# Optimization experiments

Hardware: AMD Instinct MI355X
Metric: run time of the kernel (lower is better)

Reference implementation:

```python
import jax, jax.numpy as jnp
import numpy as np

N_NODES = 50000
N_EDGES = 1600000
H = 128
F_IN = 128
N_CLASSES = 40
N_LAYERS = 8
BETA = 0.1
C_MIN = 0.2
RESIDUAL_WEIGHT = C_MIN - BETA  # 0.1


def setup_inputs() -> dict:
    key = jax.random.key(0)
    ks = jax.random.split(key, 8)
    x = jax.random.normal(ks[0], (N_NODES, F_IN), dtype=jnp.float32)
    edge_index = jax.random.randint(ks[1], (2, N_EDGES), 0, N_NODES, dtype=jnp.int64)
    W_in = jax.random.normal(ks[2], (F_IN, H), dtype=jnp.float32) * 0.05
    b_in = jax.random.normal(ks[3], (H,), dtype=jnp.float32) * 0.05
    gcn_W = jax.random.normal(ks[4], (N_LAYERS, H, H), dtype=jnp.float32) * 0.05
    srelu_b = jax.random.normal(ks[5], (N_LAYERS, H), dtype=jnp.float32) * 0.05
    W_out = jax.random.normal(ks[6], (H, N_CLASSES), dtype=jnp.float32) * 0.05
    b_out = jax.random.normal(ks[7], (N_CLASSES,), dtype=jnp.float32) * 0.05
    return {"x": x, "edge_index": edge_index, "W_in": W_in, "b_in": b_in,
            "gcn_W": gcn_W, "srelu_b": srelu_b, "W_out": W_out, "b_out": b_out}


def _gcn_norm(edge_index, num_nodes, dtype):
    # add_remaining_self_loops: drop existing self loops (zero their weight,
    # keeping static shapes) and append a full set of self loops with weight 1.
    row, col = edge_index[0], edge_index[1]
    w = jnp.where(row == col, 0.0, 1.0).astype(dtype)
    loops = jnp.arange(num_nodes, dtype=edge_index.dtype)
    row_f = jnp.concatenate([row, loops])
    col_f = jnp.concatenate([col, loops])
    w_f = jnp.concatenate([w, jnp.ones((num_nodes,), dtype=dtype)])
    deg = jax.ops.segment_sum(w_f, row_f, num_segments=num_nodes)
    deg_inv_sqrt = jnp.where(deg > 0, deg, 1.0) ** -0.5
    deg_inv_sqrt = jnp.where(deg > 0, deg_inv_sqrt, 0.0)
    norm = deg_inv_sqrt[row_f] * w_f * deg_inv_sqrt[col_f]
    return row_f, col_f, norm


def reference(x, edge_index, W_in, b_in, gcn_W, srelu_b, W_out, b_out):
    n = x.shape[0]
    row_f, col_f, norm = _gcn_norm(edge_index, n, x.dtype)
    # input layer (eval mode: dropout is identity)
    h = jax.nn.relu(x @ W_in + b_in)
    x0 = h

    def layer(h, params):
        W, sb = params
        # degree-normalized gather -> scale -> scatter_add (aggr='add')
        agg = jax.ops.segment_sum(norm[:, None] * h[row_f], col_f, num_segments=n)
        h2 = (1.0 - RESIDUAL_WEIGHT - BETA) * agg + RESIDUAL_WEIGHT * h + BETA * x0
        h2 = h2 @ W
        # SReLU: relu(x - b) + b
        h2 = jax.nn.relu(h2 - sb) + sb
        return h2, None

    h, _ = jax.lax.scan(layer, h, (gcn_W, srelu_b))
    return h @ W_out + b_out
```

## Files before the change

kernel.cpp:

```cpp
#include <hip/hip_runtime.h>

#define N_NODES 50000
#define N_EDGES 1600000
#define HDIM 128
#define N_CLASSES 40
#define N_LAYERS 8
#define CAP 128

#define BUILD_BLOCKS 782
#define CONV_BLOCKS  3125
#define PREP_BLOCKS   600

typedef _Float16 f16;
typedef _Float16 f16x2 __attribute__((ext_vector_type(2)));
typedef _Float16 f16x4 __attribute__((ext_vector_type(4)));
typedef _Float16 f16x8 __attribute__((ext_vector_type(8)));
typedef float f32x4 __attribute__((ext_vector_type(4)));
typedef int i32x4 __attribute__((ext_vector_type(4)));

__device__ __forceinline__ int clamp_idx(int v) {
    v = v < 0 ? 0 : v;
    return v >= N_NODES ? N_NODES - 1 : v;
}


__global__ __launch_bounds__(256) void setup_kernel(
        const int* __restrict__ ei, const float* __restrict__ x,
        const float* __restrict__ W_in, const float* __restrict__ gcn_W,
        const float* __restrict__ W_out,
        int* __restrict__ deg_cnt, int* __restrict__ col_cnt,
        unsigned short* __restrict__ e_slot,
        f16* __restrict__ x16, f16* __restrict__ wt, f16* __restrict__ wot) {
    int b = blockIdx.x;
    if (b < BUILD_BLOCKS) {
        int t = b * 256 + threadIdx.x;
        if (t < N_EDGES / 8) {
            i32x4 ra = ((const i32x4*)ei)[2 * t];
            i32x4 rb = ((const i32x4*)ei)[2 * t + 1];
            i32x4 ca = ((const i32x4*)(ei + N_EDGES))[2 * t];
            i32x4 cb = ((const i32x4*)(ei + N_EDGES))[2 * t + 1];
            int rs[8] = {ra[0], ra[1], ra[2], ra[3], rb[0], rb[1], rb[2], rb[3]};
            int cs[8] = {ca[0], ca[1], ca[2], ca[3], cb[0], cb[1], cb[2], cb[3]};
#pragma unroll
            for (int i = 0; i < 8; ++i) {
                int r = clamp_idx(rs[i]);
                int c = clamp_idx(cs[i]);
                if (r != c) {
                    atomicAdd(&deg_cnt[r], 1);
                    int s = atomicAdd(&col_cnt[c], 1);
                    if (s < CAP) e_slot[(size_t)c * CAP + s] = (unsigned short)r;
                }
            }
        }
    } else if (b < BUILD_BLOCKS + CONV_BLOCKS) {
        int i = (b - BUILD_BLOCKS) * 256 + threadIdx.x;
        if (i < N_NODES * HDIM / 8) {
            const float4* xs = (const float4*)x;
            float4 v0 = xs[2 * i], v1 = xs[2 * i + 1];
            f16x8 o;
            o[0] = (f16)v0.x; o[1] = (f16)v0.y; o[2] = (f16)v0.z; o[3] = (f16)v0.w;
            o[4] = (f16)v1.x; o[5] = (f16)v1.y; o[6] = (f16)v1.z; o[7] = (f16)v1.w;
            ((f16x8*)x16)[i] = o;
        }
    } else {
        int idx = (b - BUILD_BLOCKS - CONV_BLOCKS) * 256 + threadIdx.x;
        if (idx < 9 * HDIM * HDIM) {
            int mat = idx >> 14;
            int rem = idx & 16383;
            int k = rem >> 7, n = rem & 127;
            float v = (mat == 0) ? W_in[rem] : gcn_W[(mat - 1) * 16384 + rem];
            wt[mat * 16384 + n * 128 + k] = (f16)v;
        } else {
            int j = idx - 9 * HDIM * HDIM;
            if (j < 48 * 128) {
                int n = j >> 7, k = j & 127;
                wot[n * 128 + k] = (n < N_CLASSES) ? (f16)W_out[k * N_CLASSES + n] : (f16)0.f;
            }
        }
    }
}

__global__ void combo_kernel(const int* __restrict__ deg_cnt, float4* __restrict__ combo) {
    int i = blockIdx.x * blockDim.x + threadIdx.x;
    if (i >= N_NODES) return;
    float d = (float)(deg_cnt[i] + 1);
    float dis = rsqrtf(d);
    float g = sqrtf(d);
    combo[i] = make_float4(dis, 0.8f * dis, (0.8f / d + 0.1f) * g, g);
}


__global__ __launch_bounds__(256) void agg_combine(
        const f16* __restrict__ hs, const f16* __restrict__ h0_16,
        const int* __restrict__ col_cnt, const unsigned short* __restrict__ e_slot,
        const float4* __restrict__ combo, f16* __restrict__ p16) {
    int w = (blockIdx.x * blockDim.x + threadIdx.x) >> 6;
    int lane = threadIdx.x & 63;
    if (w >= N_NODES) return;
    int cnt = col_cnt[w]; if (cnt > CAP) cnt = CAP;
    const f16x2* hp = (const f16x2*)hs;
    const unsigned short* slots = e_slot + (size_t)w * CAP;
    float ax = 0.f, ay = 0.f;
    int e = 0;
    for (; e + 8 <= cnt; e += 8) {
        ushort4 sa = *(const ushort4*)(slots + e);
        ushort4 sb = *(const ushort4*)(slots + e + 4);
        f16x2 v0 = hp[(size_t)sa.x * 64 + lane];
        f16x2 v1 = hp[(size_t)sa.y * 64 + lane];
        f16x2 v2 = hp[(size_t)sa.z * 64 + lane];
        f16x2 v3 = hp[(size_t)sa.w * 64 + lane];
        f16x2 v4 = hp[(size_t)sb.x * 64 + lane];
        f16x2 v5 = hp[(size_t)sb.y * 64 + lane];
        f16x2 v6 = hp[(size_t)sb.z * 64 + lane];
        f16x2 v7 = hp[(size_t)sb.w * 64 + lane];
        ax += (float)v0[0] + (float)v1[0] + (float)v2[0] + (float)v3[0]
            + (float)v4[0] + (float)v5[0] + (float)v6[0] + (float)v7[0];
        ay += (float)v0[1] + (float)v1[1] + (float)v2[1] + (float)v3[1]
            + (float)v4[1] + (float)v5[1] + (float)v6[1] + (float)v7[1];
    }
    for (; e + 4 <= cnt; e += 4) {
        ushort4 s4 = *(const ushort4*)(slots + e);
        f16x2 v0 = hp[(size_t)s4.x * 64 + lane];
        f16x2 v1 = hp[(size_t)s4.y * 64 + lane];
        f16x2 v2 = hp[(size_t)s4.z * 64 + lane];
        f16x2 v3 = hp[(size_t)s4.w * 64 + lane];
        ax += (float)v0[0] + (float)v1[0] + (float)v2[0] + (float)v3[0];
        ay += (float)v0[1] + (float)v1[1] + (float)v2[1] + (float)v3[1];
    }
    for (; e < cnt; ++e) {
        int r = slots[e];
        f16x2 v = hp[(size_t)r * 64 + lane];
        ax += (float)v[0];
        ay += (float)v[1];
    }
    float4 cb = combo[w];
    f16x2 hw = hp[(size_t)w * 64 + lane];
    f16x2 h0v = ((const f16x2*)h0_16)[(size_t)w * 64 + lane];
    float px = cb.y * ax + cb.z * (float)hw[0] + 0.1f * (float)h0v[0];
    float py = cb.y * ay + cb.z * (float)hw[1] + 0.1f * (float)h0v[1];
    f16x2 o; o[0] = (f16)px; o[1] = (f16)py;
    ((f16x2*)p16)[(size_t)w * 64 + lane] = o;
}

#define WT_OFF 16384

__global__ __launch_bounds__(256, 2) void gemm_mfma(
        const f16* __restrict__ A, const f16* __restrict__ Wt,
        const float* __restrict__ bvec, const float4* __restrict__ combo,
        f16* __restrict__ hs_out, f16* __restrict__ h0_out, int mode) {
    __shared__ uint4 smem4[3072];
    char* smem = (char*)smem4;
    int tid = threadIdx.x;
    int r0 = blockIdx.x * 64;

    const uint4* Asrc = (const uint4*)A;
    for (int c = tid; c < 1024; c += 256) {
        int row = c >> 4, q = c & 15;
        int grow = r0 + row; if (grow >= N_NODES) grow = N_NODES - 1;
        uint4 v = Asrc[(size_t)grow * 16 + q];
        *(uint4*)&smem[row * 256 + ((q * 16) ^ ((row & 7) << 4))] = v;
    }
    const uint4* Wsrc = (const uint4*)Wt;
    for (int c = tid; c < 2048; c += 256) {
        int n = c >> 4, q = c & 15;
        uint4 v = Wsrc[n * 16 + q];
        *(uint4*)&smem[WT_OFF + n * 256 + ((q * 16) ^ ((n & 7) << 4))] = v;
    }
    __syncthreads();

    int l = tid & 63, w = tid >> 6;
    int wr = w >> 1, wc = w & 1;
    int lg = l >> 4, lm = l & 15;

    union F8 { f16x8 v8; struct { f16x4 lo, hi; } p; };
    f32x4 acc[2][4];
#pragma unroll
    for (int m = 0; m < 2; ++m)
#pragma unroll
        for (int j = 0; j < 4; ++j) acc[m][j] = (f32x4){0.f, 0.f, 0.f, 0.f};

#pragma unroll
    for (int kk = 0; kk < 4; ++kk) {
        int boff = kk * 64 + lg * 8;
        F8 a[2], b[4];
#pragma unroll
        for (int m = 0; m < 2; ++m) {
            int row = wr * 32 + m * 16 + lm;
            int swz = (row & 7) << 4;
            int rb = row * 256;
            a[m].p.lo = *(const f16x4*)&smem[rb + (boff ^ swz)];
            a[m].p.hi = *(const f16x4*)&smem[rb + ((boff + 32) ^ swz)];
        }
#pragma unroll
        for (int j = 0; j < 4; ++j) {
            int n = wc * 64 + j * 16 + lm;
            int swz = (n & 7) << 4;
            int nb = WT_OFF + n * 256;
            b[j].p.lo = *(const f16x4*)&smem[nb + (boff ^ swz)];
            b[j].p.hi = *(const f16x4*)&smem[nb + ((boff + 32) ^ swz)];
        }
#pragma unroll
        for (int m = 0; m < 2; ++m)
#pragma unroll
            for (int j = 0; j < 4; ++j)
                acc[m][j] = __builtin_amdgcn_mfma_f32_16x16x32_f16(a[m].v8, b[j].v8, acc[m][j], 0, 0, 0);
    }

#pragma unroll
    for (int m = 0; m < 2; ++m) {
#pragma unroll
        for (int r = 0; r < 4; ++r) {
            int row = r0 + wr * 32 + m * 16 + lg * 4 + r;
            if (row < N_NODES) {
                float dis = combo[row].x;
#pragma unroll
                for (int j = 0; j < 4; ++j) {
                    int col = wc * 64 + j * 16 + lm;
                    float bias = bvec[col];
                    float v = acc[m][j][r];
                    v = mode ? fmaxf(v, bias) : fmaxf(v + bias, 0.f);
                    if (mode == 0) h0_out[(size_t)row * HDIM + col] = (f16)v;
                    hs_out[(size_t)row * HDIM + col] = (f16)(dis * v);
                }
            }
        }
    }
}

#define WOT_OFF 16384

__global__ __launch_bounds__(256) void out_mfma(
        const f16* __restrict__ A, const f16* __restrict__ Wot,
        const float* __restrict__ bo, const float4* __restrict__ combo,
        float* __restrict__ out) {
    __shared__ uint4 smem4[1792];
    char* smem = (char*)smem4;
    int tid = threadIdx.x;
    int r0 = blockIdx.x * 64;

    const uint4* Asrc = (const uint4*)A;
    for (int c = tid; c < 1024; c += 256) {
        int row = c >> 4, q = c & 15;
        int grow = r0 + row; if (grow >= N_NODES) grow = N_NODES - 1;
        uint4 v = Asrc[(size_t)grow * 16 + q];
        *(uint4*)&smem[row * 256 + ((q * 16) ^ ((row & 7) << 4))] = v;
    }
    const uint4* Wsrc = (const uint4*)Wot;
    for (int c = tid; c < 768; c += 256) {
        int n = c >> 4, q = c & 15;
        uint4 v = Wsrc[n * 16 + q];
        *(uint4*)&smem[WOT_OFF + n * 256 + ((q * 16) ^ ((n & 7) << 4))] = v;
    }
    __syncthreads();

    int l = tid & 63, w = tid >> 6;
    int lg = l >> 4, lm = l & 15;

    union F8 { f16x8 v8; struct { f16x4 lo, hi; } p; };
    f32x4 acc[3];
#pragma unroll
    for (int j = 0; j < 3; ++j) acc[j] = (f32x4){0.f, 0.f, 0.f, 0.f};

#pragma unroll
    for (int kk = 0; kk < 4; ++kk) {
        int boff = kk * 64 + lg * 8;
        F8 a, b[3];
        int row = w * 16 + lm;
        int swz = (row & 7) << 4;
        int rb = row * 256;
        a.p.lo = *(const f16x4*)&smem[rb + (boff ^ swz)];
        a.p.hi = *(const f16x4*)&smem[rb + ((boff + 32) ^ swz)];
#pragma unroll
        for (int j = 0; j < 3; ++j) {
            int n = j * 16 + lm;
            int swz2 = (n & 7) << 4;
            int nb = WOT_OFF + n * 256;
            b[j].p.lo = *(const f16x4*)&smem[nb + (boff ^ swz2)];
            b[j].p.hi = *(const f16x4*)&smem[nb + ((boff + 32) ^ swz2)];
        }
#pragma unroll
        for (int j = 0; j < 3; ++j)
            acc[j] = __builtin_amdgcn_mfma_f32_16x16x32_f16(a.v8, b[j].v8, acc[j], 0, 0, 0);
    }

#pragma unroll
    for (int r = 0; r < 4; ++r) {
        int row = r0 + w * 16 + lg * 4 + r;
        if (row < N_NODES) {
            float g2 = combo[row].w;
#pragma unroll
            for (int j = 0; j < 3; ++j) {
                int col = j * 16 + lm;
                if (col < N_CLASSES)
                    out[(size_t)row * N_CLASSES + col] = g2 * acc[j][r] + bo[col];
            }
        }
    }
}


extern "C" void kernel_launch(void* const* d_in, const int* in_sizes, int n_in,
                              void* d_out, int out_size, void* d_ws, size_t ws_size,
                              hipStream_t stream) {
    const float* x       = (const float*)d_in[0];
    const int*   ei      = (const int*)d_in[1];
    const float* W_in    = (const float*)d_in[2];
    const float* b_in    = (const float*)d_in[3];
    const float* gcn_W   = (const float*)d_in[4];
    const float* srelu_b = (const float*)d_in[5];
    const float* W_out   = (const float*)d_in[6];
    const float* b_out   = (const float*)d_in[7];
    float* outp = (float*)d_out;

    char* ws = (char*)d_ws;
    size_t off = 0;
    auto alloc = [&](size_t bytes) -> void* {
        void* p = ws + off;
        off += (bytes + 255) & ~(size_t)255;
        return p;
    };
    int*    deg_cnt = (int*)alloc((size_t)N_NODES * 4);
    int*    col_cnt = (int*)alloc((size_t)N_NODES * 4);
    float4* combo   = (float4*)alloc((size_t)N_NODES * 16);
    unsigned short* e_slot = (unsigned short*)alloc((size_t)N_NODES * CAP * 2);
    f16*    wt16    = (f16*)alloc((size_t)9 * HDIM * HDIM * 2);
    f16*    wot16   = (f16*)alloc((size_t)48 * HDIM * 2);
    f16*    x16     = (f16*)alloc((size_t)N_NODES * HDIM * 2);
    f16*    h0_16   = (f16*)alloc((size_t)N_NODES * HDIM * 2);
    f16*    hs0     = (f16*)alloc((size_t)N_NODES * HDIM * 2);
    f16*    hsA     = (f16*)alloc((size_t)N_NODES * HDIM * 2);
    f16*    hsB     = (f16*)alloc((size_t)N_NODES * HDIM * 2);
    f16*    p16     = (f16*)alloc((size_t)N_NODES * HDIM * 2);

    hipMemsetAsync(deg_cnt, 0, (size_t)N_NODES * 4, stream);
    hipMemsetAsync(col_cnt, 0, (size_t)N_NODES * 4, stream);

    setup_kernel<<<BUILD_BLOCKS + CONV_BLOCKS + PREP_BLOCKS, 256, 0, stream>>>(
        ei, x, W_in, gcn_W, W_out, deg_cnt, col_cnt, e_slot, x16, wt16, wot16);
    combo_kernel<<<(N_NODES + 255) / 256, 256, 0, stream>>>(deg_cnt, combo);

    gemm_mfma<<<(N_NODES + 63) / 64, 256, 0, stream>>>(
        x16, wt16, b_in, combo, hs0, h0_16, 0);

    const f16* hcur = hs0;
    for (int l = 0; l < N_LAYERS; ++l) {
        f16* hnext = (l & 1) ? hsB : hsA;
        agg_combine<<<(N_NODES * 64 + 255) / 256, 256, 0, stream>>>(
            hcur, h0_16, col_cnt, e_slot, combo, p16);
        gemm_mfma<<<(N_NODES + 63) / 64, 256, 0, stream>>>(
            p16, wt16 + (size_t)(l + 1) * HDIM * HDIM,
            srelu_b + (size_t)l * HDIM, combo, hnext, nullptr, 1);
        hcur = hnext;
    }

    out_mfma<<<(N_NODES + 63) / 64, 256, 0, stream>>>(hcur, wot16, b_out, combo, outp);
}
```

Measured before the change: 773.2 us.

## Fuse aggregation with layer GEMM and input projection into setup kernel

Each layer's gather-aggregate-combine now writes its 64-row tile straight into shared memory and feeds the MFMA GEMM in the same kernel. This removes the intermediate p16 buffer round-trip and one launch per layer. The input projection is folded into the setup kernel, converting x and W_in to fp16 on the fly, and a new kernel computes degree coefficients and the scaled h0. The trade-off is that each wave now gathers 16 nodes serially with fewer resident waves, which may reduce memory-latency hiding in the gather.

```diff
diff --git a/kernel.cpp b/kernel.cpp
--- a/kernel.cpp
+++ b/kernel.cpp
@@ -8,8 +8,9 @@
 #define CAP 128
 
 #define BUILD_BLOCKS 782
-#define CONV_BLOCKS  3125
-#define PREP_BLOCKS   600
+#define PREP_BLOCKS  600
+#define GEMM0_BLOCKS 782
+#define WT_OFF 16384
 
 typedef _Float16 f16;
 typedef _Float16 f16x2 __attribute__((ext_vector_type(2)));
@@ -26,14 +27,18 @@
 
 __global__ __launch_bounds__(256) void setup_kernel(
         const int* __restrict__ ei, const float* __restrict__ x,
-        const float* __restrict__ W_in, const float* __restrict__ gcn_W,
-        const float* __restrict__ W_out,
+        const float* __restrict__ W_in, const float* __restrict__ b_in,
+        const float* __restrict__ gcn_W, const float* __restrict__ W_out,
         int* __restrict__ deg_cnt, int* __restrict__ col_cnt,
         unsigned short* __restrict__ e_slot,
-        f16* __restrict__ x16, f16* __restrict__ wt, f16* __restrict__ wot) {
+        f16* __restrict__ wt, f16* __restrict__ wot, f16* __restrict__ h0_out) {
+    __shared__ uint4 smem4[3072];
+    char* smem = (char*)smem4;
     int b = blockIdx.x;
+    int tid = threadIdx.x;
+
     if (b < BUILD_BLOCKS) {
-        int t = b * 256 + threadIdx.x;
+        int t = b * 256 + tid;
         if (t < N_EDGES / 8) {
             i32x4 ra = ((const i32x4*)ei)[2 * t];
             i32x4 rb = ((const i32x4*)ei)[2 * t + 1];
@@ -52,18 +57,10 @@
                 }
             }
         }
-    } else if (b < BUILD_BLOCKS + CONV_BLOCKS) {
-        int i = (b - BUILD_BLOCKS) * 256 + threadIdx.x;
-        if (i < N_NODES * HDIM / 8) {
-            const float4* xs = (const float4*)x;
-            float4 v0 = xs[2 * i], v1 = xs[2 * i + 1];
-            f16x8 o;
-            o[0] = (f16)v0.x; o[1] = (f16)v0.y; o[2] = (f16)v0.z; o[3] = (f16)v0.w;
-            o[4] = (f16)v1.x; o[5] = (f16)v1.y; o[6] = (f16)v1.z; o[7] = (f16)v1.w;
-            ((f16x8*)x16)[i] = o;
-        }
-    } else {
-        int idx = (b - BUILD_BLOCKS - CONV_BLOCKS) * 256 + threadIdx.x;
+        return;
+    }
+    if (b < BUILD_BLOCKS + PREP_BLOCKS) {
+        int idx = (b - BUILD_BLOCKS) * 256 + tid;
         if (idx < 9 * HDIM * HDIM) {
             int mat = idx >> 14;
             int rem = idx & 16383;
@@ -77,112 +74,41 @@
                 wot[n * 128 + k] = (n < N_CLASSES) ? (f16)W_out[k * N_CLASSES + n] : (f16)0.f;
             }
         }
-    }
-}
-
-__global__ void combo_kernel(const int* __restrict__ deg_cnt, float4* __restrict__ combo) {
-    int i = blockIdx.x * blockDim.x + threadIdx.x;
-    if (i >= N_NODES) return;
-    float d = (float)(deg_cnt[i] + 1);
-    float dis = rsqrtf(d);
-    float g = sqrtf(d);
-    combo[i] = make_float4(dis, 0.8f * dis, (0.8f / d + 0.1f) * g, g);
-}
-
-
-__global__ __launch_bounds__(256) void agg_combine(
-        const f16* __restrict__ hs, const f16* __restrict__ h0_16,
-        const int* __restrict__ col_cnt, const unsigned short* __restrict__ e_slot,
-        const float4* __restrict__ combo, f16* __restrict__ p16) {
-    int w = (blockIdx.x * blockDim.x + threadIdx.x) >> 6;
-    int lane = threadIdx.x & 63;
-    if (w >= N_NODES) return;
-    int cnt = col_cnt[w]; if (cnt > CAP) cnt = CAP;
-    const f16x2* hp = (const f16x2*)hs;
-    const unsigned short* slots = e_slot + (size_t)w * CAP;
-    float ax = 0.f, ay = 0.f;
-    int e = 0;
-    for (; e + 8 <= cnt; e += 8) {
-        ushort4 sa = *(const ushort4*)(slots + e);
-        ushort4 sb = *(const ushort4*)(slots + e + 4);
-        f16x2 v0 = hp[(size_t)sa.x * 64 + lane];
-        f16x2 v1 = hp[(size_t)sa.y * 64 + lane];
-        f16x2 v2 = hp[(size_t)sa.z * 64 + lane];
-        f16x2 v3 = hp[(size_t)sa.w * 64 + lane];
-        f16x2 v4 = hp[(size_t)sb.x * 64 + lane];
-        f16x2 v5 = hp[(size_t)sb.y * 64 + lane];
-        f16x2 v6 = hp[(size_t)sb.z * 64 + lane];
-        f16x2 v7 = hp[(size_t)sb.w * 64 + lane];
-        ax += (float)v0[0] + (float)v1[0] + (float)v2[0] + (float)v3[0]
-            + (float)v4[0] + (float)v5[0] + (float)v6[0] + (float)v7[0];
-        ay += (float)v0[1] + (float)v1[1] + (float)v2[1] + (float)v3[1]
-            + (float)v4[1] + (float)v5[1] + (float)v6[1] + (float)v7[1];
-    }
-    for (; e + 4 <= cnt; e += 4) {
-        ushort4 s4 = *(const ushort4*)(slots + e);
-        f16x2 v0 = hp[(size_t)s4.x * 64 + lane];
-        f16x2 v1 = hp[(size_t)s4.y * 64 + lane];
-        f16x2 v2 = hp[(size_t)s4.z * 64 + lane];
-        f16x2 v3 = hp[(size_t)s4.w * 64 + lane];
-        ax += (float)v0[0] + (float)v1[0] + (float)v2[0] + (float)v3[0];
-        ay += (float)v0[1] + (float)v1[1] + (float)v2[1] + (float)v3[1];
-    }
-    for (; e < cnt; ++e) {
-        int r = slots[e];
-        f16x2 v = hp[(size_t)r * 64 + lane];
-        ax += (float)v[0];
-        ay += (float)v[1];
-    }
-    float4 cb = combo[w];
-    f16x2 hw = hp[(size_t)w * 64 + lane];
-    f16x2 h0v = ((const f16x2*)h0_16)[(size_t)w * 64 + lane];
-    float px = cb.y * ax + cb.z * (float)hw[0] + 0.1f * (float)h0v[0];
-    float py = cb.y * ay + cb.z * (float)hw[1] + 0.1f * (float)h0v[1];
-    f16x2 o; o[0] = (f16)px; o[1] = (f16)py;
-    ((f16x2*)p16)[(size_t)w * 64 + lane] = o;
-}
-
-#define WT_OFF 16384
-
-__global__ __launch_bounds__(256, 2) void gemm_mfma(
-        const f16* __restrict__ A, const f16* __restrict__ Wt,
-        const float* __restrict__ bvec, const float4* __restrict__ combo,
-        f16* __restrict__ hs_out, f16* __restrict__ h0_out, int mode) {
-    __shared__ uint4 smem4[3072];
-    char* smem = (char*)smem4;
-    int tid = threadIdx.x;
-    int r0 = blockIdx.x * 64;
-
-    const uint4* Asrc = (const uint4*)A;
-    for (int c = tid; c < 1024; c += 256) {
-        int row = c >> 4, q = c & 15;
+        return;
+    }
+
+    int r0 = (b - BUILD_BLOCKS - PREP_BLOCKS) * 64;
+
+    const float4* x4 = (const float4*)x;
+    for (int c = tid; c < 2048; c += 256) {
+        int row = c >> 5, f4 = c & 31;
         int grow = r0 + row; if (grow >= N_NODES) grow = N_NODES - 1;
-        uint4 v = Asrc[(size_t)grow * 16 + q];
-        *(uint4*)&smem[row * 256 + ((q * 16) ^ ((row & 7) << 4))] = v;
-    }
-    const uint4* Wsrc = (const uint4*)Wt;
-    for (int c = tid; c < 2048; c += 256) {
-        int n = c >> 4, q = c & 15;
-        uint4 v = Wsrc[n * 16 + q];
-        *(uint4*)&smem[WT_OFF + n * 256 + ((q * 16) ^ ((n & 7) << 4))] = v;
+        float4 v = x4[(size_t)grow * 32 + f4];
+        f16x4 h; h[0] = (f16)v.x; h[1] = (f16)v.y; h[2] = (f16)v.z; h[3] = (f16)v.w;
+        int addr = row * 256 + ((((f4 >> 1) << 4) ^ ((row & 7) << 4)) + (f4 & 1) * 8);
+        *(f16x4*)&smem[addr] = h;
+    }
+    for (int idx = tid; idx < 16384; idx += 256) {
+        int k = idx >> 7, n = idx & 127;
+        float v = W_in[k * 128 + n];
+        int addr = WT_OFF + n * 256 + ((((k >> 3) << 4) ^ ((n & 7) << 4)) + (k & 7) * 2);
+        *(f16*)&smem[addr] = (f16)v;
     }
     __syncthreads();
 
     int l = tid & 63, w = tid >> 6;
     int wr = w >> 1, wc = w & 1;
     int lg = l >> 4, lm = l & 15;
-
     union F8 { f16x8 v8; struct { f16x4 lo, hi; } p; };
     f32x4 acc[2][4];
 #pragma unroll
     for (int m = 0; m < 2; ++m)
 #pragma unroll
         for (int j = 0; j < 4; ++j) acc[m][j] = (f32x4){0.f, 0.f, 0.f, 0.f};
-
 #pragma unroll
     for (int kk = 0; kk < 4; ++kk) {
         int boff = kk * 64 + lg * 8;
-        F8 a[2], b[4];
+        F8 a[2], bb[4];
 #pragma unroll
         for (int m = 0; m < 2; ++m) {
             int row = wr * 32 + m * 16 + lm;
@@ -196,16 +122,154 @@
             int n = wc * 64 + j * 16 + lm;
             int swz = (n & 7) << 4;
             int nb = WT_OFF + n * 256;
-            b[j].p.lo = *(const f16x4*)&smem[nb + (boff ^ swz)];
-            b[j].p.hi = *(const f16x4*)&smem[nb + ((boff + 32) ^ swz)];
+            bb[j].p.lo = *(const f16x4*)&smem[nb + (boff ^ swz)];
+            bb[j].p.hi = *(const f16x4*)&smem[nb + ((boff + 32) ^ swz)];
         }
 #pragma unroll
         for (int m = 0; m < 2; ++m)
 #pragma unroll
             for (int j = 0; j < 4; ++j)
-                acc[m][j] = __builtin_amdgcn_mfma_f32_16x16x32_f16(a[m].v8, b[j].v8, acc[m][j], 0, 0, 0);
-    }
-
+                acc[m][j] = __builtin_amdgcn_mfma_f32_16x16x32_f16(a[m].v8, bb[j].v8, acc[m][j], 0, 0, 0);
+    }
+#pragma unroll
+    for (int m = 0; m < 2; ++m) {
+#pragma unroll
+        for (int r = 0; r < 4; ++r) {
+            int row = r0 + wr * 32 + m * 16 + lg * 4 + r;
+            if (row < N_NODES) {
+#pragma unroll
+                for (int j = 0; j < 4; ++j) {
+                    int col = wc * 64 + j * 16 + lm;
+                    float v = fmaxf(acc[m][j][r] + b_in[col], 0.f);
+                    h0_out[(size_t)row * HDIM + col] = (f16)v;
+                }
+            }
+        }
+    }
+}
+
+__global__ __launch_bounds__(256) void combo_scale(
+        const int* __restrict__ deg_cnt, const f16* __restrict__ h0,
+        float4* __restrict__ combo, f16* __restrict__ hs0) {
+    int node = blockIdx.x * 4 + (threadIdx.x >> 6);
+    int lane = threadIdx.x & 63;
+    if (node >= N_NODES) return;
+    float d = (float)(deg_cnt[node] + 1);
+    float dis = rsqrtf(d);
+    float g = sqrtf(d);
+    if (lane == 0) combo[node] = make_float4(dis, 0.8f * dis, (0.8f / d + 0.1f) * g, g);
+    f16x2 h = ((const f16x2*)h0)[(size_t)node * 64 + lane];
+    f16x2 o; o[0] = (f16)(dis * (float)h[0]); o[1] = (f16)(dis * (float)h[1]);
+    ((f16x2*)hs0)[(size_t)node * 64 + lane] = o;
+}
+
+
+__global__ __launch_bounds__(256, 3) void layer_fused(
+        const f16* __restrict__ hs, const f16* __restrict__ h0_16,
+        const int* __restrict__ col_cnt, const unsigned short* __restrict__ e_slot,
+        const float4* __restrict__ combo, const f16* __restrict__ Wt,
+        const float* __restrict__ sb, f16* __restrict__ hs_out) {
+    __shared__ uint4 smem4[3072];
+    char* smem = (char*)smem4;
+    int tid = threadIdx.x;
+    int lane = tid & 63, w4 = tid >> 6;
+    int r0 = blockIdx.x * 64;
+
+    const uint4* Wsrc = (const uint4*)Wt;
+    for (int c = tid; c < 2048; c += 256) {
+        int n = c >> 4, q = c & 15;
+        uint4 v = Wsrc[n * 16 + q];
+        *(uint4*)&smem[WT_OFF + n * 256 + ((q * 16) ^ ((n & 7) << 4))] = v;
+    }
+
+    const f16x2* hp = (const f16x2*)hs;
+    int chunk = (lane >> 2) << 4;
+    int sub = (lane & 3) << 2;
+    for (int t = 0; t < 16; ++t) {
+        int row = w4 * 16 + t;
+        int node = r0 + row;
+        float px = 0.f, py = 0.f;
+        if (node < N_NODES) {
+            int cnt = col_cnt[node]; if (cnt > CAP) cnt = CAP;
+            const unsigned short* slots = e_slot + (size_t)node * CAP;
+            float ax = 0.f, ay = 0.f;
+            int e = 0;
+            for (; e + 8 <= cnt; e += 8) {
+                ushort4 sa = *(const ushort4*)(slots + e);
+                ushort4 sbv = *(const ushort4*)(slots + e + 4);
+                f16x2 v0 = hp[(size_t)sa.x * 64 + lane];
+                f16x2 v1 = hp[(size_t)sa.y * 64 + lane];
+                f16x2 v2 = hp[(size_t)sa.z * 64 + lane];
+                f16x2 v3 = hp[(size_t)sa.w * 64 + lane];
+                f16x2 v4 = hp[(size_t)sbv.x * 64 + lane];
+                f16x2 v5 = hp[(size_t)sbv.y * 64 + lane];
+                f16x2 v6 = hp[(size_t)sbv.z * 64 + lane];
+                f16x2 v7 = hp[(size_t)sbv.w * 64 + lane];
+                ax += (float)v0[0] + (float)v1[0] + (float)v2[0] + (float)v3[0]
+                    + (float)v4[0] + (float)v5[0] + (float)v6[0] + (float)v7[0];
+                ay += (float)v0[1] + (float)v1[1] + (float)v2[1] + (float)v3[1]
+                    + (float)v4[1] + (float)v5[1] + (float)v6[1] + (float)v7[1];
+            }
+            for (; e + 4 <= cnt; e += 4) {
+                ushort4 s4 = *(const ushort4*)(slots + e);
+                f16x2 v0 = hp[(size_t)s4.x * 64 + lane];
+                f16x2 v1 = hp[(size_t)s4.y * 64 + lane];
+                f16x2 v2 = hp[(size_t)s4.z * 64 + lane];
+                f16x2 v3 = hp[(size_t)s4.w * 64 + lane];
+                ax += (float)v0[0] + (float)v1[0] + (float)v2[0] + (float)v3[0];
+                ay += (float)v0[1] + (float)v1[1] + (float)v2[1] + (float)v3[1];
+            }
+            for (; e < cnt; ++e) {
+                int r = slots[e];
+                f16x2 v = hp[(size_t)r * 64 + lane];
+                ax += (float)v[0];
+                ay += (float)v[1];
+            }
+            float4 cb = combo[node];
+            f16x2 hw = hp[(size_t)node * 64 + lane];
+            f16x2 h0v = ((const f16x2*)h0_16)[(size_t)node * 64 + lane];
+            px = cb.y * ax + cb.z * (float)hw[0] + 0.1f * (float)h0v[0];
+            py = cb.y * ay + cb.z * (float)hw[1] + 0.1f * (float)h0v[1];
+        }
+        f16x2 o; o[0] = (f16)px; o[1] = (f16)py;
+        *(f16x2*)&smem[row * 256 + (chunk ^ ((row & 7) << 4)) + sub] = o;
+    }
+    __syncthreads();
+
+    int wr = w4 >> 1, wc = w4 & 1;
+    int lg = lane >> 4, lm = lane & 15;
+    union F8 { f16x8 v8; struct { f16x4 lo, hi; } p; };
+    f32x4 acc[2][4];
+#pragma unroll
+    for (int m = 0; m < 2; ++m)
+#pragma unroll
+        for (int j = 0; j < 4; ++j) acc[m][j] = (f32x4){0.f, 0.f, 0.f, 0.f};
+#pragma unroll
+    for (int kk = 0; kk < 4; ++kk) {
+        int boff = kk * 64 + lg * 8;
+        F8 a[2], bb[4];
+#pragma unroll
+        for (int m = 0; m < 2; ++m) {
+            int row = wr * 32 + m * 16 + lm;
+            int swz = (row & 7) << 4;
+            int rb = row * 256;
+            a[m].p.lo = *(const f16x4*)&smem[rb + (boff ^ swz)];
+            a[m].p.hi = *(const f16x4*)&smem[rb + ((boff + 32) ^ swz)];
+        }
+#pragma unroll
+        for (int j = 0; j < 4; ++j) {
+            int n = wc * 64 + j * 16 + lm;
+            int swz = (n & 7) << 4;
+            int nb = WT_OFF + n * 256;
+            bb[j].p.lo = *(const f16x4*)&smem[nb + (boff ^ swz)];
+            bb[j].p.hi = *(const f16x4*)&smem[nb + ((boff + 32) ^ swz)];
+        }
+#pragma unroll
+        for (int m = 0; m < 2; ++m)
+#pragma unroll
+            for (int j = 0; j < 4; ++j)
+                acc[m][j] = __builtin_amdgcn_mfma_f32_16x16x32_f16(a[m].v8, bb[j].v8, acc[m][j], 0, 0, 0);
+    }
 #pragma unroll
     for (int m = 0; m < 2; ++m) {
 #pragma unroll
@@ -216,10 +280,7 @@
 #pragma unroll
                 for (int j = 0; j < 4; ++j) {
                     int col = wc * 64 + j * 16 + lm;
-                    float bias = bvec[col];
-                    float v = acc[m][j][r];
-                    v = mode ? fmaxf(v, bias) : fmaxf(v + bias, 0.f);
-                    if (mode == 0) h0_out[(size_t)row * HDIM + col] = (f16)v;
+                    float v = fmaxf(acc[m][j][r], sb[col]);
                     hs_out[(size_t)row * HDIM + col] = (f16)(dis * v);
                 }
             }
@@ -325,31 +386,24 @@
     unsigned short* e_slot = (unsigned short*)alloc((size_t)N_NODES * CAP * 2);
     f16*    wt16    = (f16*)alloc((size_t)9 * HDIM * HDIM * 2);
     f16*    wot16   = (f16*)alloc((size_t)48 * HDIM * 2);
-    f16*    x16     = (f16*)alloc((size_t)N_NODES * HDIM * 2);
     f16*    h0_16   = (f16*)alloc((size_t)N_NODES * HDIM * 2);
     f16*    hs0     = (f16*)alloc((size_t)N_NODES * HDIM * 2);
     f16*    hsA     = (f16*)alloc((size_t)N_NODES * HDIM * 2);
     f16*    hsB     = (f16*)alloc((size_t)N_NODES * HDIM * 2);
-    f16*    p16     = (f16*)alloc((size_t)N_NODES * HDIM * 2);
 
     hipMemsetAsync(deg_cnt, 0, (size_t)N_NODES * 4, stream);
     hipMemsetAsync(col_cnt, 0, (size_t)N_NODES * 4, stream);
 
-    setup_kernel<<<BUILD_BLOCKS + CONV_BLOCKS + PREP_BLOCKS, 256, 0, stream>>>(
-        ei, x, W_in, gcn_W, W_out, deg_cnt, col_cnt, e_slot, x16, wt16, wot16);
-    combo_kernel<<<(N_NODES + 255) / 256, 256, 0, stream>>>(deg_cnt, combo);
-
-    gemm_mfma<<<(N_NODES + 63) / 64, 256, 0, stream>>>(
-        x16, wt16, b_in, combo, hs0, h0_16, 0);
+    setup_kernel<<<BUILD_BLOCKS + PREP_BLOCKS + GEMM0_BLOCKS, 256, 0, stream>>>(
+        ei, x, W_in, b_in, gcn_W, W_out, deg_cnt, col_cnt, e_slot, wt16, wot16, h0_16);
+    combo_scale<<<(N_NODES + 3) / 4, 256, 0, stream>>>(deg_cnt, h0_16, combo, hs0);
 
     const f16* hcur = hs0;
     for (int l = 0; l < N_LAYERS; ++l) {
         f16* hnext = (l & 1) ? hsB : hsA;
-        agg_combine<<<(N_NODES * 64 + 255) / 256, 256, 0, stream>>>(
-            hcur, h0_16, col_cnt, e_slot, combo, p16);
-        gemm_mfma<<<(N_NODES + 63) / 64, 256, 0, stream>>>(
-            p16, wt16 + (size_t)(l + 1) * HDIM * HDIM,
-            srelu_b + (size_t)l * HDIM, combo, hnext, nullptr, 1);
+        layer_fused<<<(N_NODES + 63) / 64, 256, 0, stream>>>(
+            hcur, h0_16, col_cnt, e_slot, combo,
+            wt16 + (size_t)(l + 1) * HDIM * HDIM, srelu_b + (size_t)l * HDIM, hnext);
         hcur = hnext;
     }
 
```

Result: slower. 1.368 ms (+76.9%).
